# Performance work log

Measured on AMD Instinct MI355X. Metric: run time of the kernel, lower is better.

The kernel has to match this reference:

```python
import jax, jax.numpy as jnp
import numpy as np

N_NODES = 60000
N_EDGES = 240000
F_IN = 768
F_OUT = 128
HEADS = 6
LRELU_SLOPE = 0.2


def _gat_layer(x, edge_index, W, a_src, a_tgt, skip_W, bias, concat, activate):
    # x: (N, F_in); W/skip_W: (F_in, H*F); a_src/a_tgt: (H, F)
    N = x.shape[0]
    H, F = a_src.shape
    proj = (x @ W).reshape(N, H, F)                      # (N,H,F)
    s_src = jnp.einsum('nhf,hf->nh', proj, a_src)        # (N,H)
    s_tgt = jnp.einsum('nhf,hf->nh', proj, a_tgt)        # (N,H)
    src, tgt = edge_index[0], edge_index[1]
    e = jax.nn.leaky_relu(s_src[src] + s_tgt[tgt], LRELU_SLOPE)   # (E,H)
    # neighborhood-wise (per target node) stable softmax
    e_max = jax.ops.segment_max(e, tgt, num_segments=N)
    e = jnp.exp(e - e_max[tgt])
    denom = jax.ops.segment_sum(e, tgt, num_segments=N)
    alpha = e / (denom[tgt] + 1e-16)                     # (E,H)
    msg = proj[src] * alpha[:, :, None]                  # (E,H,F)
    out = jax.ops.segment_sum(msg, tgt, num_segments=N)  # (N,H,F)
    # skip connection (F != F_in so skip projection is used)
    out = out + (x @ skip_W).reshape(N, H, F)
    out = out.reshape(N, H * F) if concat else out.mean(axis=1)
    out = out + bias
    return jax.nn.elu(out) if activate else out


def setup_inputs() -> dict:
    key = jax.random.key(0)
    ks = jax.random.split(key, 20)
    d = {}
    d['x'] = jax.random.normal(ks[0], (N_NODES, F_IN), dtype=jnp.float32)
    d['edge_index'] = jax.random.randint(ks[1], (2, N_EDGES), 0, N_NODES, dtype=jnp.int32)
    HF = HEADS * F_OUT  # 768
    s = 1.0 / np.sqrt(F_IN)
    for l in range(3):
        d[f'W{l}'] = jax.random.normal(ks[2 + 5 * l], (F_IN, HF), dtype=jnp.float32) * s
        d[f'a_src{l}'] = jax.random.normal(ks[3 + 5 * l], (HEADS, F_OUT), dtype=jnp.float32) * 0.1
        d[f'a_tgt{l}'] = jax.random.normal(ks[4 + 5 * l], (HEADS, F_OUT), dtype=jnp.float32) * 0.1
        d[f'skip{l}'] = jax.random.normal(ks[5 + 5 * l], (F_IN, HF), dtype=jnp.float32) * s
        d[f'b{l}'] = jnp.zeros((HF if l < 2 else F_OUT,), dtype=jnp.float32)
    return d


def reference(x, W0, a_src0, a_tgt0, skip0, b0,
              W1, a_src1, a_tgt1, skip1, b1,
              W2, a_src2, a_tgt2, skip2, b2, edge_index):
    h = _gat_layer(x, edge_index, W0, a_src0, a_tgt0, skip0, b0, concat=True, activate=True)
    h = _gat_layer(h, edge_index, W1, a_src1, a_tgt1, skip1, b1, concat=True, activate=True)
    h = _gat_layer(h, edge_index, W2, a_src2, a_tgt2, skip2, b2, concat=False, activate=False)
    return h
```

## Files before the change

### kernel.cpp

```cpp
#include <hip/hip_runtime.h>
#include <stdint.h>

#define NODES 60000
#define NPAD  60032
#define EDGES 240000
#define KDIM  768
#define HF    768
#define FOUT  128
#define SCAN_B 59

typedef unsigned short u16;
typedef __bf16 bf16x8 __attribute__((ext_vector_type(8)));
typedef float f32x4 __attribute__((ext_vector_type(4)));

__device__ __forceinline__ float bf2f(u16 u) {
  union { uint32_t i; float f; } v; v.i = ((uint32_t)u) << 16; return v.f;
}
__device__ __forceinline__ u16 f2bf(float f) {
  union { float f; uint32_t i; } v; v.f = f;
  return (u16)((v.i + 0x7FFF + ((v.i >> 16) & 1)) >> 16);
}

__global__ __launch_bounds__(256) void convert_x_k(const float* __restrict__ x, u16* __restrict__ xb) {
  const size_t g = ((size_t)blockIdx.x * 256 + threadIdx.x) * 4;
  if (g >= (size_t)NPAD * KDIM) return;
  ushort4 o;
  if (g < (size_t)NODES * KDIM) {
    const float4 v = *(const float4*)(x + g);
    o.x = f2bf(v.x); o.y = f2bf(v.y); o.z = f2bf(v.z); o.w = f2bf(v.w);
  } else { o.x = o.y = o.z = o.w = 0; }
  *(ushort4*)(xb + g) = o;
}

template <int MODE>
__global__ __launch_bounds__(256) void prep_wcat_k(const float* __restrict__ W, const float* __restrict__ SK,
                                                   u16* __restrict__ WT) {
  __shared__ u16 tile[32][33];
  const int n0 = blockIdx.x * 32, k0 = blockIdx.y * 32;
  const int tx = threadIdx.x & 31, ty = threadIdx.x >> 5;
#pragma unroll
  for (int r = 0; r < 32; r += 8) {
    const int k = k0 + ty + r, n = n0 + tx;
    float v;
    if (n < HF) {
      v = W[(size_t)k * HF + n];
    } else if (MODE == 0) {
      v = SK[(size_t)k * HF + (n - HF)];
    } else {
      const int f = n - HF;
      v = 0.f;
#pragma unroll
      for (int h = 0; h < 6; ++h) v += SK[(size_t)k * HF + h * FOUT + f];
      v *= (1.0f / 6.0f);
    }
    tile[ty + r][tx] = f2bf(v);
  }
  __syncthreads();
#pragma unroll
  for (int r = 0; r < 32; r += 8) {
    const int n = n0 + ty + r, k = k0 + tx;
    WT[(size_t)n * KDIM + k] = tile[tx][ty + r];
  }
}

__global__ __launch_bounds__(256) void hist_k(const int* __restrict__ tgt, int* __restrict__ deg) {
  const int e = blockIdx.x * 256 + threadIdx.x;
  if (e < EDGES) atomicAdd(&deg[tgt[e]], 1);
}

__global__ __launch_bounds__(1024) void scan1_k(const int* __restrict__ deg, int* __restrict__ rp,
                                                int* __restrict__ partial) {
  __shared__ int buf[1024];
  const int tid = threadIdx.x;
  const int i = blockIdx.x * 1024 + tid;
  const int v = (i < NODES) ? deg[i] : 0;
  buf[tid] = v;
  __syncthreads();
  for (int off = 1; off < 1024; off <<= 1) {
    const int t = (tid >= off) ? buf[tid - off] : 0;
    __syncthreads();
    buf[tid] += t;
    __syncthreads();
  }
  if (i < NODES) rp[i] = buf[tid] - v;
  if (tid == 1023) partial[blockIdx.x] = buf[1023];
}

__global__ __launch_bounds__(64) void scan2_k(int* __restrict__ partial, int* __restrict__ rpN) {
  __shared__ int buf[64];
  const int tid = threadIdx.x;
  const int v = (tid < SCAN_B) ? partial[tid] : 0;
  buf[tid] = v;
  __syncthreads();
  for (int off = 1; off < 64; off <<= 1) {
    const int t = (tid >= off) ? buf[tid - off] : 0;
    __syncthreads();
    buf[tid] += t;
    __syncthreads();
  }
  if (tid < SCAN_B) partial[tid] = buf[tid] - v;
  if (tid == 63) *rpN = buf[63];
}

__global__ __launch_bounds__(1024) void scan3_k(int* __restrict__ rp, const int* __restrict__ partial,
                                                int* __restrict__ cur) {
  const int i = blockIdx.x * 1024 + threadIdx.x;
  if (i < NODES) {
    const int v = rp[i] + partial[blockIdx.x];
    rp[i] = v;
    cur[i] = v;
  }
}

__global__ __launch_bounds__(256) void scatter_k(const int* __restrict__ srcv, const int* __restrict__ tgt,
                                                 int* __restrict__ cur, int* __restrict__ esrc) {
  const int e = blockIdx.x * 256 + threadIdx.x;
  if (e < EDGES) {
    const int t = tgt[e];
    const int pos = atomicAdd(&cur[t], 1);
    esrc[pos] = srcv[e];
  }
}

__global__ __launch_bounds__(256) void attn_k(const int* __restrict__ rp, const int* __restrict__ esrc,
                                              const float* __restrict__ ss, const float* __restrict__ stg,
                                              float* __restrict__ alp, float* __restrict__ invd) {
  const int t = blockIdx.x * 256 + threadIdx.x;
  if (t >= NODES) return;
  const int b = rp[t], e = rp[t + 1];
  float sth[6], m[6], d[6];
#pragma unroll
  for (int h = 0; h < 6; ++h) { sth[h] = stg[t * 6 + h]; m[h] = -1e30f; d[h] = 0.f; }
  for (int j = b; j < e; ++j) {
    const int s = esrc[j];
#pragma unroll
    for (int h = 0; h < 6; ++h) {
      float sc = ss[s * 6 + h] + sth[h];
      sc = sc > 0.f ? sc : 0.2f * sc;
      m[h] = fmaxf(m[h], sc);
    }
  }
  for (int j = b; j < e; ++j) {
    const int s = esrc[j];
#pragma unroll
    for (int h = 0; h < 6; ++h) {
      float sc = ss[s * 6 + h] + sth[h];
      sc = sc > 0.f ? sc : 0.2f * sc;
      const float ev = expf(sc - m[h]);
      d[h] += ev;
      alp[(size_t)j * 6 + h] = ev;
    }
  }
#pragma unroll
  for (int h = 0; h < 6; ++h) invd[t * 6 + h] = 1.f / (d[h] + 1e-16f);
}

__global__ __launch_bounds__(256, 4) void gemm_k(const u16* __restrict__ A, const u16* __restrict__ BT,
                                                 u16* __restrict__ C,
                                                 const float* __restrict__ a_src, const float* __restrict__ a_tgt,
                                                 float* __restrict__ ss, float* __restrict__ stg,
                                                 int nbx, int ncat) {
  __shared__ u16 As[2][4096];
  __shared__ u16 Bs[2][4096];
  float* sp = (float*)&As[0][0];
  const int tid = threadIdx.x;
  const int lane = tid & 63;
  const int w = tid >> 6;
  const int wm = w >> 1, wn = w & 1;
  const int r16 = lane & 15, g4 = lane >> 4;

  const int NWG = nbx * 469;
  const int q = NWG >> 3, rr = NWG & 7;
  const int orig = blockIdx.x;
  const int xcd = orig & 7, idx = orig >> 3;
  const int wg = (xcd < rr ? xcd * (q + 1) : rr * (q + 1) + (xcd - rr) * q) + idx;
  const int bx = wg % nbx, by = wg / nbx;

  const size_t rowBase = (size_t)by * 128;
  const int colBase = bx * 128;

  const int c0 = tid, c1 = tid + 256;
  const size_t aoff0 = (rowBase + (c0 >> 2)) * KDIM + (c0 & 3) * 8;
  const size_t aoff1 = (rowBase + (c1 >> 2)) * KDIM + (c1 & 3) * 8;
  const size_t boff0 = ((size_t)(colBase + (c0 >> 2))) * KDIM + (c0 & 3) * 8;
  const size_t boff1 = ((size_t)(colBase + (c1 >> 2))) * KDIM + (c1 & 3) * 8;

  auto stage = [&](int buf, int k0) {
    __builtin_amdgcn_global_load_lds((__attribute__((address_space(1))) void*)(A + aoff0 + k0),
                                     (__attribute__((address_space(3))) void*)(&As[buf][w * 512]), 16, 0, 0);
    __builtin_amdgcn_global_load_lds((__attribute__((address_space(1))) void*)(A + aoff1 + k0),
                                     (__attribute__((address_space(3))) void*)(&As[buf][2048 + w * 512]), 16, 0, 0);
    __builtin_amdgcn_global_load_lds((__attribute__((address_space(1))) void*)(BT + boff0 + k0),
                                     (__attribute__((address_space(3))) void*)(&Bs[buf][w * 512]), 16, 0, 0);
    __builtin_amdgcn_global_load_lds((__attribute__((address_space(1))) void*)(BT + boff1 + k0),
                                     (__attribute__((address_space(3))) void*)(&Bs[buf][2048 + w * 512]), 16, 0, 0);
  };

  f32x4 acc[4][4];
#pragma unroll
  for (int i = 0; i < 4; ++i)
#pragma unroll
    for (int j = 0; j < 4; ++j) acc[i][j] = f32x4{0.f, 0.f, 0.f, 0.f};

  stage(0, 0);
  __syncthreads();
  for (int ks = 0; ks < 24; ++ks) {
    const int buf = ks & 1;
    if (ks < 23) stage(buf ^ 1, (ks + 1) * 32);
    bf16x8 af[4], bv[4];
#pragma unroll
    for (int i = 0; i < 4; ++i)
      af[i] = *(const bf16x8*)(&As[buf][(wm * 64 + i * 16 + r16) * 32 + g4 * 8]);
#pragma unroll
    for (int j = 0; j < 4; ++j)
      bv[j] = *(const bf16x8*)(&Bs[buf][(wn * 64 + j * 16 + r16) * 32 + g4 * 8]);
#pragma unroll
    for (int i = 0; i < 4; ++i)
#pragma unroll
      for (int j = 0; j < 4; ++j)
        acc[i][j] = __builtin_amdgcn_mfma_f32_16x16x32_bf16(af[i], bv[j], acc[i][j], 0, 0, 0);
    __syncthreads();
  }

#pragma unroll
  for (int i = 0; i < 4; ++i) {
    const size_t row0 = rowBase + wm * 64 + i * 16 + g4 * 4;
#pragma unroll
    for (int j = 0; j < 4; ++j) {
      const int col = colBase + wn * 64 + j * 16 + r16;
#pragma unroll
      for (int r = 0; r < 4; ++r)
        C[(row0 + r) * ncat + col] = f2bf(acc[i][j][r]);
    }
  }

  if (bx < 6) {
#pragma unroll
    for (int pass = 0; pass < 2; ++pass) {
      const float* av = (pass == 0) ? a_src : a_tgt;
      float a4[4];
#pragma unroll
      for (int j = 0; j < 4; ++j) a4[j] = av[bx * FOUT + wn * 64 + j * 16 + r16];
#pragma unroll
      for (int i = 0; i < 4; ++i) {
#pragma unroll
        for (int r = 0; r < 4; ++r) {
          float p = 0.f;
#pragma unroll
          for (int j = 0; j < 4; ++j) p += acc[i][j][r] * a4[j];
#pragma unroll
          for (int off = 1; off < 16; off <<= 1) p += __shfl_xor(p, off, 64);
          if (r16 == 0) {
            const int row = wm * 64 + i * 16 + g4 * 4 + r;
            sp[pass * 256 + wn * 128 + row] = p;
          }
        }
      }
    }
    __syncthreads();
    if (tid < 128) {
      const size_t row = rowBase + tid;
      if (row < NODES) {
        ss[row * 6 + bx] = sp[tid] + sp[128 + tid];
        stg[row * 6 + bx] = sp[256 + tid] + sp[384 + tid];
      }
    }
  }
}

template <int MODE>
__global__ __launch_bounds__(256) void aggregate_k(const u16* __restrict__ Cb, const int* __restrict__ rp,
                                                   const int* __restrict__ esrc, const float* __restrict__ alp,
                                                   const float* __restrict__ invd, const float* __restrict__ bias,
                                                   u16* __restrict__ xnext, float* __restrict__ outf) {
  constexpr int ncat = (MODE == 0) ? 1536 : 896;
  const int t = blockIdx.x * 4 + (threadIdx.x >> 6);
  const int lane = threadIdx.x & 63;
  if (t >= NODES) return;
  const int l4 = lane * 4;
  const int h0 = lane >> 5;
  float macc[3][4];
#pragma unroll
  for (int k = 0; k < 3; ++k)
#pragma unroll
    for (int c = 0; c < 4; ++c) macc[k][c] = 0.f;

  const int b = rp[t], e = rp[t + 1];
  int j = b;
  for (; j + 1 < e; j += 2) {
    const int s0 = esrc[j], s1 = esrc[j + 1];
    const float2 p0 = *(const float2*)(alp + (size_t)j * 6);
    const float2 p1 = *(const float2*)(alp + (size_t)j * 6 + 2);
    const float2 p2 = *(const float2*)(alp + (size_t)j * 6 + 4);
    const float2 q0 = *(const float2*)(alp + (size_t)(j + 1) * 6);
    const float2 q1 = *(const float2*)(alp + (size_t)(j + 1) * 6 + 2);
    const float2 q2 = *(const float2*)(alp + (size_t)(j + 1) * 6 + 4);
    const float a0[6] = {p0.x, p0.y, p1.x, p1.y, p2.x, p2.y};
    const float a1[6] = {q0.x, q0.y, q1.x, q1.y, q2.x, q2.y};
    const u16* pr0 = Cb + (size_t)s0 * ncat;
    const u16* pr1 = Cb + (size_t)s1 * ncat;
#pragma unroll
    for (int k = 0; k < 3; ++k) {
      const ushort4 v0 = *(const ushort4*)(pr0 + l4 + 256 * k);
      const ushort4 v1 = *(const ushort4*)(pr1 + l4 + 256 * k);
      const float aa0 = a0[h0 + 2 * k], aa1 = a1[h0 + 2 * k];
      macc[k][0] += aa0 * bf2f(v0.x) + aa1 * bf2f(v1.x);
      macc[k][1] += aa0 * bf2f(v0.y) + aa1 * bf2f(v1.y);
      macc[k][2] += aa0 * bf2f(v0.z) + aa1 * bf2f(v1.z);
      macc[k][3] += aa0 * bf2f(v0.w) + aa1 * bf2f(v1.w);
    }
  }
  if (j < e) {
    const int s0 = esrc[j];
    const float2 p0 = *(const float2*)(alp + (size_t)j * 6);
    const float2 p1 = *(const float2*)(alp + (size_t)j * 6 + 2);
    const float2 p2 = *(const float2*)(alp + (size_t)j * 6 + 4);
    const float a0[6] = {p0.x, p0.y, p1.x, p1.y, p2.x, p2.y};
    const u16* pr0 = Cb + (size_t)s0 * ncat;
#pragma unroll
    for (int k = 0; k < 3; ++k) {
      const ushort4 v0 = *(const ushort4*)(pr0 + l4 + 256 * k);
      const float aa0 = a0[h0 + 2 * k];
      macc[k][0] += aa0 * bf2f(v0.x);
      macc[k][1] += aa0 * bf2f(v0.y);
      macc[k][2] += aa0 * bf2f(v0.z);
      macc[k][3] += aa0 * bf2f(v0.w);
    }
  }

  float inv[3];
#pragma unroll
  for (int k = 0; k < 3; ++k) inv[k] = invd[t * 6 + h0 + 2 * k];

  if (MODE == 0) {
    const u16* sk = Cb + (size_t)t * ncat + HF;
#pragma unroll
    for (int k = 0; k < 3; ++k) {
      const ushort4 s4 = *(const ushort4*)(sk + l4 + 256 * k);
      ushort4 o;
      float v0 = macc[k][0] * inv[k] + bf2f(s4.x) + bias[l4 + 256 * k];
      float v1 = macc[k][1] * inv[k] + bf2f(s4.y) + bias[l4 + 256 * k + 1];
      float v2 = macc[k][2] * inv[k] + bf2f(s4.z) + bias[l4 + 256 * k + 2];
      float v3 = macc[k][3] * inv[k] + bf2f(s4.w) + bias[l4 + 256 * k + 3];
      o.x = f2bf(v0 > 0.f ? v0 : expm1f(v0));
      o.y = f2bf(v1 > 0.f ? v1 : expm1f(v1));
      o.z = f2bf(v2 > 0.f ? v2 : expm1f(v2));
      o.w = f2bf(v3 > 0.f ? v3 : expm1f(v3));
      *(ushort4*)(xnext + (size_t)t * HF + l4 + 256 * k) = o;
    }
  } else {
    float4 o;
    float* op = &o.x;
#pragma unroll
    for (int c = 0; c < 4; ++c) {
      const float s3 = macc[0][c] * inv[0] + macc[1][c] * inv[1] + macc[2][c] * inv[2];
      const float tot = s3 + __shfl_xor(s3, 32, 64);
      op[c] = tot * (1.0f / 6.0f);
    }
    if (lane < 32) {
      const int f = lane * 4;
      const ushort4 s4 = *(const ushort4*)(Cb + (size_t)t * ncat + HF + f);
      o.x += bf2f(s4.x) + bias[f];
      o.y += bf2f(s4.y) + bias[f + 1];
      o.z += bf2f(s4.z) + bias[f + 2];
      o.w += bf2f(s4.w) + bias[f + 3];
      *(float4*)(outf + (size_t)t * FOUT + f) = o;
    }
  }
}

#define OFF_XBF 0ull
#define OFF_CB  92209152ull
#define OFF_WT  276627456ull
#define OFF_SS  279023616ull
#define OFF_ST  280463616ull
#define OFF_ALP 281903616ull
#define OFF_RP  287663616ull
#define OFF_CUR 287903744ull
#define OFF_ESR 288143872ull

extern "C" void kernel_launch(void* const* d_in, const int* in_sizes, int n_in,
                              void* d_out, int out_size, void* d_ws, size_t ws_size,
                              hipStream_t stream) {
  const float* x = (const float*)d_in[0];
  const int ei = (in_sizes[1] == 2 * EDGES) ? 1 : 16;
  const int base = (ei == 1) ? 2 : 1;
  const float *W[3], *AS[3], *AT[3], *SK[3], *B[3];
  for (int l = 0; l < 3; ++l) {
    W[l]  = (const float*)d_in[base + 5 * l + 0];
    AS[l] = (const float*)d_in[base + 5 * l + 1];
    AT[l] = (const float*)d_in[base + 5 * l + 2];
    SK[l] = (const float*)d_in[base + 5 * l + 3];
    B[l]  = (const float*)d_in[base + 5 * l + 4];
  }
  const int* edges = (const int*)d_in[ei];
  const int* srcv = edges;
  const int* tgtv = edges + EDGES;
  float* out = (float*)d_out;

  char* ws = (char*)d_ws;
  u16* xbf = (u16*)(ws + OFF_XBF);
  u16* Cb  = (u16*)(ws + OFF_CB);
  u16* WT  = (u16*)(ws + OFF_WT);
  float* invd = (float*)(ws + OFF_WT);
  int* partial = (int*)(ws + OFF_WT);
  float* ss  = (float*)(ws + OFF_SS);
  float* stg = (float*)(ws + OFF_ST);
  float* alp = (float*)(ws + OFF_ALP);
  int* rp  = (int*)(ws + OFF_RP);
  int* cur = (int*)(ws + OFF_CUR);
  int* esr = (int*)(ws + OFF_ESR);

  hipMemsetAsync(cur, 0, NODES * sizeof(int), stream);
  hist_k<<<(EDGES + 255) / 256, 256, 0, stream>>>(tgtv, cur);
  scan1_k<<<SCAN_B, 1024, 0, stream>>>(cur, rp, partial);
  scan2_k<<<1, 64, 0, stream>>>(partial, rp + NODES);
  scan3_k<<<SCAN_B, 1024, 0, stream>>>(rp, partial, cur);
  scatter_k<<<(EDGES + 255) / 256, 256, 0, stream>>>(srcv, tgtv, cur, esr);

  convert_x_k<<<45024, 256, 0, stream>>>(x, xbf);

  for (int l = 0; l < 3; ++l) {
    const int nbx = (l < 2) ? 12 : 7;
    const int ncat = nbx * 128;
    if (l < 2)
      prep_wcat_k<0><<<dim3(48, 24), 256, 0, stream>>>(W[l], SK[l], WT);
    else
      prep_wcat_k<1><<<dim3(28, 24), 256, 0, stream>>>(W[l], SK[l], WT);
    gemm_k<<<nbx * 469, 256, 0, stream>>>(xbf, WT, Cb, AS[l], AT[l], ss, stg, nbx, ncat);
    attn_k<<<(NODES + 255) / 256, 256, 0, stream>>>(rp, esr, ss, stg, alp, invd);
    if (l < 2)
      aggregate_k<0><<<15000, 256, 0, stream>>>(Cb, rp, esr, alp, invd, B[l], xbf, nullptr);
    else
      aggregate_k<1><<<15000, 256, 0, stream>>>(Cb, rp, esr, alp, invd, B[l], nullptr, out);
  }
}
```

Before: 903.8 us.

## Fuse attention softmax into aggregation kernel, dropping attn_k and alpha buffer

Removes the separate per-node attention kernel and its alpha/inverse-denominator buffers. Each wavefront in the aggregation kernel now computes the per-head max over its neighborhood, then recomputes the exponentials on the fly while accumulating messages and the denominator. This saves one launch per layer plus the write and re-read of the edge-by-head alpha array. The cost is redundant score and exp work across lanes, a switch to the faster, less precise __expf, and an extra pass over the edge source indices.

```diff
diff --git a/kernel.cpp b/kernel.cpp
--- a/kernel.cpp
+++ b/kernel.cpp
@@ -120,39 +120,6 @@
     const int pos = atomicAdd(&cur[t], 1);
     esrc[pos] = srcv[e];
   }
-}
-
-__global__ __launch_bounds__(256) void attn_k(const int* __restrict__ rp, const int* __restrict__ esrc,
-                                              const float* __restrict__ ss, const float* __restrict__ stg,
-                                              float* __restrict__ alp, float* __restrict__ invd) {
-  const int t = blockIdx.x * 256 + threadIdx.x;
-  if (t >= NODES) return;
-  const int b = rp[t], e = rp[t + 1];
-  float sth[6], m[6], d[6];
-#pragma unroll
-  for (int h = 0; h < 6; ++h) { sth[h] = stg[t * 6 + h]; m[h] = -1e30f; d[h] = 0.f; }
-  for (int j = b; j < e; ++j) {
-    const int s = esrc[j];
-#pragma unroll
-    for (int h = 0; h < 6; ++h) {
-      float sc = ss[s * 6 + h] + sth[h];
-      sc = sc > 0.f ? sc : 0.2f * sc;
-      m[h] = fmaxf(m[h], sc);
-    }
-  }
-  for (int j = b; j < e; ++j) {
-    const int s = esrc[j];
-#pragma unroll
-    for (int h = 0; h < 6; ++h) {
-      float sc = ss[s * 6 + h] + sth[h];
-      sc = sc > 0.f ? sc : 0.2f * sc;
-      const float ev = expf(sc - m[h]);
-      d[h] += ev;
-      alp[(size_t)j * 6 + h] = ev;
-    }
-  }
-#pragma unroll
-  for (int h = 0; h < 6; ++h) invd[t * 6 + h] = 1.f / (d[h] + 1e-16f);
 }
 
 __global__ __launch_bounds__(256, 4) void gemm_k(const u16* __restrict__ A, const u16* __restrict__ BT,
@@ -270,8 +237,9 @@
 
 template <int MODE>
 __global__ __launch_bounds__(256) void aggregate_k(const u16* __restrict__ Cb, const int* __restrict__ rp,
-                                                   const int* __restrict__ esrc, const float* __restrict__ alp,
-                                                   const float* __restrict__ invd, const float* __restrict__ bias,
+                                                   const int* __restrict__ esrc,
+                                                   const float* __restrict__ ss, const float* __restrict__ stg,
+                                                   const float* __restrict__ bias,
                                                    u16* __restrict__ xnext, float* __restrict__ outf) {
   constexpr int ncat = (MODE == 0) ? 1536 : 896;
   const int t = blockIdx.x * 4 + (threadIdx.x >> 6);
@@ -279,58 +247,84 @@
   if (t >= NODES) return;
   const int l4 = lane * 4;
   const int h0 = lane >> 5;
-  float macc[3][4];
-#pragma unroll
-  for (int k = 0; k < 3; ++k)
-#pragma unroll
-    for (int c = 0; c < 4; ++c) macc[k][c] = 0.f;
 
   const int b = rp[t], e = rp[t + 1];
+
+  float sth[3], m[3];
+#pragma unroll
+  for (int k = 0; k < 3; ++k) { sth[k] = stg[t * 6 + h0 + 2 * k]; m[k] = -1e30f; }
+
   int j = b;
   for (; j + 1 < e; j += 2) {
     const int s0 = esrc[j], s1 = esrc[j + 1];
-    const float2 p0 = *(const float2*)(alp + (size_t)j * 6);
-    const float2 p1 = *(const float2*)(alp + (size_t)j * 6 + 2);
-    const float2 p2 = *(const float2*)(alp + (size_t)j * 6 + 4);
-    const float2 q0 = *(const float2*)(alp + (size_t)(j + 1) * 6);
-    const float2 q1 = *(const float2*)(alp + (size_t)(j + 1) * 6 + 2);
-    const float2 q2 = *(const float2*)(alp + (size_t)(j + 1) * 6 + 4);
-    const float a0[6] = {p0.x, p0.y, p1.x, p1.y, p2.x, p2.y};
-    const float a1[6] = {q0.x, q0.y, q1.x, q1.y, q2.x, q2.y};
+#pragma unroll
+    for (int k = 0; k < 3; ++k) {
+      float sc0 = ss[s0 * 6 + h0 + 2 * k] + sth[k];
+      float sc1 = ss[s1 * 6 + h0 + 2 * k] + sth[k];
+      sc0 = sc0 > 0.f ? sc0 : 0.2f * sc0;
+      sc1 = sc1 > 0.f ? sc1 : 0.2f * sc1;
+      m[k] = fmaxf(m[k], fmaxf(sc0, sc1));
+    }
+  }
+  if (j < e) {
+    const int s0 = esrc[j];
+#pragma unroll
+    for (int k = 0; k < 3; ++k) {
+      float sc0 = ss[s0 * 6 + h0 + 2 * k] + sth[k];
+      sc0 = sc0 > 0.f ? sc0 : 0.2f * sc0;
+      m[k] = fmaxf(m[k], sc0);
+    }
+  }
+
+  float macc[3][4], d[3];
+#pragma unroll
+  for (int k = 0; k < 3; ++k) {
+    d[k] = 0.f;
+#pragma unroll
+    for (int c = 0; c < 4; ++c) macc[k][c] = 0.f;
+  }
+  j = b;
+  for (; j + 1 < e; j += 2) {
+    const int s0 = esrc[j], s1 = esrc[j + 1];
     const u16* pr0 = Cb + (size_t)s0 * ncat;
     const u16* pr1 = Cb + (size_t)s1 * ncat;
 #pragma unroll
     for (int k = 0; k < 3; ++k) {
       const ushort4 v0 = *(const ushort4*)(pr0 + l4 + 256 * k);
       const ushort4 v1 = *(const ushort4*)(pr1 + l4 + 256 * k);
-      const float aa0 = a0[h0 + 2 * k], aa1 = a1[h0 + 2 * k];
-      macc[k][0] += aa0 * bf2f(v0.x) + aa1 * bf2f(v1.x);
-      macc[k][1] += aa0 * bf2f(v0.y) + aa1 * bf2f(v1.y);
-      macc[k][2] += aa0 * bf2f(v0.z) + aa1 * bf2f(v1.z);
-      macc[k][3] += aa0 * bf2f(v0.w) + aa1 * bf2f(v1.w);
+      float sc0 = ss[s0 * 6 + h0 + 2 * k] + sth[k];
+      float sc1 = ss[s1 * 6 + h0 + 2 * k] + sth[k];
+      sc0 = sc0 > 0.f ? sc0 : 0.2f * sc0;
+      sc1 = sc1 > 0.f ? sc1 : 0.2f * sc1;
+      const float ev0 = __expf(sc0 - m[k]);
+      const float ev1 = __expf(sc1 - m[k]);
+      d[k] += ev0 + ev1;
+      macc[k][0] += ev0 * bf2f(v0.x) + ev1 * bf2f(v1.x);
+      macc[k][1] += ev0 * bf2f(v0.y) + ev1 * bf2f(v1.y);
+      macc[k][2] += ev0 * bf2f(v0.z) + ev1 * bf2f(v1.z);
+      macc[k][3] += ev0 * bf2f(v0.w) + ev1 * bf2f(v1.w);
     }
   }
   if (j < e) {
     const int s0 = esrc[j];
-    const float2 p0 = *(const float2*)(alp + (size_t)j * 6);
-    const float2 p1 = *(const float2*)(alp + (size_t)j * 6 + 2);
-    const float2 p2 = *(const float2*)(alp + (size_t)j * 6 + 4);
-    const float a0[6] = {p0.x, p0.y, p1.x, p1.y, p2.x, p2.y};
     const u16* pr0 = Cb + (size_t)s0 * ncat;
 #pragma unroll
     for (int k = 0; k < 3; ++k) {
       const ushort4 v0 = *(const ushort4*)(pr0 + l4 + 256 * k);
-      const float aa0 = a0[h0 + 2 * k];
-      macc[k][0] += aa0 * bf2f(v0.x);
-      macc[k][1] += aa0 * bf2f(v0.y);
-      macc[k][2] += aa0 * bf2f(v0.z);
-      macc[k][3] += aa0 * bf2f(v0.w);
+      float sc0 = ss[s0 * 6 + h0 + 2 * k] + sth[k];
+      sc0 = sc0 > 0.f ? sc0 : 0.2f * sc0;
+      const float ev0 = __expf(sc0 - m[k]);
+      d[k] += ev0;
+      macc[k][0] += ev0 * bf2f(v0.x);
+      macc[k][1] += ev0 * bf2f(v0.y);
+      macc[k][2] += ev0 * bf2f(v0.z);
+      macc[k][3] += ev0 * bf2f(v0.w);
     }
   }
 
   float inv[3];
 #pragma unroll
-  for (int k = 0; k < 3; ++k) inv[k] = invd[t * 6 + h0 + 2 * k];
+  for (int k = 0; k < 3; ++k) inv[k] = 1.f / (d[k] + 1e-16f);
 
   if (MODE == 0) {
     const u16* sk = Cb + (size_t)t * ncat + HF;
@@ -374,7 +368,6 @@
 #define OFF_WT  276627456ull
 #define OFF_SS  279023616ull
 #define OFF_ST  280463616ull
-#define OFF_ALP 281903616ull
 #define OFF_RP  287663616ull
 #define OFF_CUR 287903744ull
 #define OFF_ESR 288143872ull
@@ -402,11 +395,9 @@
   u16* xbf = (u16*)(ws + OFF_XBF);
   u16* Cb  = (u16*)(ws + OFF_CB);
   u16* WT  = (u16*)(ws + OFF_WT);
-  float* invd = (float*)(ws + OFF_WT);
   int* partial = (int*)(ws + OFF_WT);
   float* ss  = (float*)(ws + OFF_SS);
   float* stg = (float*)(ws + OFF_ST);
-  float* alp = (float*)(ws + OFF_ALP);
   int* rp  = (int*)(ws + OFF_RP);
   int* cur = (int*)(ws + OFF_CUR);
   int* esr = (int*)(ws + OFF_ESR);
@@ -428,10 +419,9 @@
     else
       prep_wcat_k<1><<<dim3(28, 24), 256, 0, stream>>>(W[l], SK[l], WT);
     gemm_k<<<nbx * 469, 256, 0, stream>>>(xbf, WT, Cb, AS[l], AT[l], ss, stg, nbx, ncat);
-    attn_k<<<(NODES + 255) / 256, 256, 0, stream>>>(rp, esr, ss, stg, alp, invd);
     if (l < 2)
-      aggregate_k<0><<<15000, 256, 0, stream>>>(Cb, rp, esr, alp, invd, B[l], xbf, nullptr);
+      aggregate_k<0><<<15000, 256, 0, stream>>>(Cb, rp, esr, ss, stg, B[l], xbf, nullptr);
     else
-      aggregate_k<1><<<15000, 256, 0, stream>>>(Cb, rp, esr, alp, invd, B[l], nullptr, out);
-  }
-}
+      aggregate_k<1><<<15000, 256, 0, stream>>>(Cb, rp, esr, ss, stg, B[l], nullptr, out);
+  }
+}
```

New measurement: 877.1 us. 3.0% less time.
